# Performance work log

Measured on AMD Instinct MI355X. Metric: run time of the kernel, lower is better.

Reference implementation:

```python
import jax, jax.numpy as jnp
import numpy as np

ALPHA = 1.0
EPS = 1e-6


def setup_inputs() -> dict:
    key = jax.random.key(0)
    ks = jax.random.split(key, 6)
    B, d_lat, hidden, n_genes = 256, 32, 512, 4000
    z = jax.random.normal(ks[0], (B, d_lat), dtype=jnp.float32)
    W1 = jax.random.normal(ks[1], (d_lat, hidden), dtype=jnp.float32) / np.sqrt(d_lat)
    b1 = jnp.zeros((hidden,), dtype=jnp.float32)
    W2 = jax.random.normal(ks[2], (hidden, n_genes), dtype=jnp.float32) / np.sqrt(hidden)
    b2 = jnp.zeros((n_genes,), dtype=jnp.float32)
    log_theta = 0.5 * jax.random.normal(ks[3], (n_genes,), dtype=jnp.float32)
    return {"z": z, "W1": W1, "b1": b1, "W2": W2, "b2": b2, "log_theta": log_theta}


def _decode_mu(z_vec, W1, b1, W2, b2):
    # NB decoder mean for a single latent vector; lib_dummy == 1 so no scaling.
    h = jax.nn.relu(z_vec @ W1 + b1)            # [hidden]
    return jax.nn.softplus(h @ W2 + b2)          # [n_genes]


def reference(z, W1, b1, W2, b2, log_theta):
    d_lat = z.shape[1]
    theta = jnp.exp(log_theta)                   # [G], per-gene dispersion

    f = lambda zv: _decode_mu(zv, W1, b1, W2, b2)

    mu = jax.vmap(f)(z)                          # [B, G]
    J = jax.vmap(jax.jacfwd(f))(z)               # [B, G, d_lat]

    # weights computed under no_grad in the original
    mu_ng = jax.lax.stop_gradient(mu)
    weights = theta / (mu_ng * (mu_ng + theta) + EPS)   # [B, G]

    # Gram[b, i, j] = sum_g J[b,g,i] * w[b,g] * J[b,g,j]  (== U @ U.T with U = sqrt(w)*J^T)
    Gram = jnp.einsum('bgi,bg,bgj->bij', J, weights, J)  # [B, d_lat, d_lat]

    eye = jnp.eye(d_lat, dtype=z.dtype)
    losses = jnp.sum((Gram - ALPHA * eye) ** 2, axis=(1, 2))  # [B]
    return jnp.mean(losses)
```

## Files before the change

### kernel.cpp

```cpp
#include <hip/hip_runtime.h>

typedef __bf16 bf16x8 __attribute__((ext_vector_type(8)));
typedef float f32x4 __attribute__((ext_vector_type(4)));
typedef unsigned short u16x8 __attribute__((ext_vector_type(8)));

typedef const void __attribute__((address_space(1)))* gas_ptr;
typedef void __attribute__((address_space(3)))* las_ptr;

#define GLOAD16(gp, lp) __builtin_amdgcn_global_load_lds((gas_ptr)(gp), (las_ptr)(lp), 16, 0, 0)

__device__ __forceinline__ unsigned short f2bf(float f) {
  unsigned int u = __float_as_uint(f);
  u += 0x7FFF + ((u >> 16) & 1);
  return (unsigned short)(u >> 16);
}
__device__ __forceinline__ float bf2f(unsigned short u) {
  return __uint_as_float(((unsigned int)u) << 16);
}

__global__ __launch_bounds__(256) void k_w2t(const float* __restrict__ W2,
                                             unsigned short* __restrict__ W2T) {
  __shared__ float tile[64][65];
  const int gt = blockIdx.x;
  const int jt = blockIdx.y;
  const int t = threadIdx.x;
  const int c = t & 63, r4 = t >> 6;
#pragma unroll
  for (int r = 0; r < 16; ++r) {
    int jj = r * 4 + r4;
    int g = gt * 64 + c;
    tile[jj][c] = (g < 4000) ? W2[(size_t)(jt * 64 + jj) * 4000 + g] : 0.f;
  }
  __syncthreads();
#pragma unroll
  for (int r = 0; r < 16; ++r) {
    int gg = r * 4 + r4;
    W2T[(size_t)(gt * 64 + gg) * 512 + jt * 64 + c] = f2bf(tile[c][gg]);
  }
}

__global__ __launch_bounds__(256) void k_maskprep(const float* __restrict__ z,
                                                  const float* __restrict__ W1,
                                                  const float* __restrict__ b1,
                                                  unsigned short* __restrict__ Hb,
                                                  unsigned short* __restrict__ Astack) {
  __shared__ float zs[32];
  __shared__ __align__(8) unsigned char mk[512];
  const int b = blockIdx.x, t = threadIdx.x;
  if (t < 32) zs[t] = z[b * 32 + t];
  __syncthreads();
#pragma unroll
  for (int jj = 0; jj < 2; ++jj) {
    int j = t + jj * 256;
    float a = b1[j];
#pragma unroll
    for (int i = 0; i < 32; ++i) a = fmaf(zs[i], W1[i * 512 + j], a);
    bool m = a > 0.f;
    mk[j] = m ? 1 : 0;
    Hb[b * 512 + j] = m ? f2bf(a) : (unsigned short)0;
  }
  __syncthreads();
#pragma unroll
  for (int k = 0; k < 8; ++k) {
    int c8 = t + k * 256;
    int row = c8 >> 6;
    int k8 = (c8 & 63) * 8;
    unsigned long long m8 = *(const unsigned long long*)(mk + k8);
    const float* w = W1 + row * 512 + k8;
    u16x8 out;
#pragma unroll
    for (int e = 0; e < 8; ++e)
      out[e] = ((m8 >> (e * 8)) & 0xffULL) ? f2bf(w[e]) : (unsigned short)0;
    *(u16x8*)(Astack + ((size_t)(b * 32 + row)) * 512 + k8) = out;
  }
}

__global__ __launch_bounds__(512, 2) void k_gemm(const unsigned short* __restrict__ Astack,
                                                 const unsigned short* __restrict__ W2T,
                                                 const unsigned short* __restrict__ Hb,
                                                 const float* __restrict__ b2,
                                                 const float* __restrict__ log_theta,
                                                 float* __restrict__ Gram) {
  extern __shared__ __align__(16) char smem[];

  const int bm = blockIdx.x;
  const int g0 = blockIdx.y * 256;
  const int t = threadIdx.x;
  const int lane = t & 63;
  const int wave = t >> 6;
  const int wm = wave >> 2;
  const int wn = wave & 3;
  const int trow = t >> 3;
  const int kxor = (((t & 7) ^ (trow & 7)) << 3);
  const int c16 = lane & 15;
  const int lg = lane >> 4;

  f32x4 acc[8][4];
#pragma unroll
  for (int mt = 0; mt < 8; ++mt)
#pragma unroll
    for (int nt = 0; nt < 4; ++nt) acc[mt][nt] = (f32x4){0.f, 0.f, 0.f, 0.f};
  f32x4 sacc[4];
#pragma unroll
  for (int nt = 0; nt < 4; ++nt) sacc[nt] = (f32x4){0.f, 0.f, 0.f, 0.f};

  const unsigned short* Aptr = Astack + (size_t)bm * 256 * 512;
  const unsigned short* Bptr = W2T + (size_t)g0 * 512;
  char* H_lds = smem + 139264;

#define STAGE_BIG(buf, kt)                                                            \
  do {                                                                                \
    _Pragma("unroll") for (int q = 0; q < 4; ++q)                                     \
      GLOAD16(Aptr + (size_t)(q * 64 + trow) * 512 + (kt) * 64 + kxor,                \
              smem + (buf) * 65536 + q * 8192 + wave * 1024);                         \
    _Pragma("unroll") for (int q = 0; q < 4; ++q)                                     \
      GLOAD16(Bptr + (size_t)(q * 64 + trow) * 512 + (kt) * 64 + kxor,                \
              smem + (buf) * 65536 + 32768 + q * 8192 + wave * 1024);                 \
  } while (0)

  STAGE_BIG(0, 0);

#pragma unroll
  for (int i = 0; i < 2; ++i) {
    int o = t * 2 + i;
    int row = o >> 6;
    int col8 = (o & 63) * 8;
    u16x8 v;
    if (row < 8) {
      v = *(const u16x8*)(Hb + (size_t)(bm * 8 + row) * 512 + col8);
    } else {
#pragma unroll
      for (int e = 0; e < 8; ++e) v[e] = 0;
    }
    *(u16x8*)(H_lds + row * 1024 + ((col8 * 2) ^ ((row & 7) << 4))) = v;
  }
  __syncthreads();

  for (int kt = 0; kt < 8; ++kt) {
    int cur = kt & 1;
    if (kt < 7) STAGE_BIG(cur ^ 1, kt + 1);
    const char* Ab = smem + cur * 65536;
    const char* Bb = smem + cur * 65536 + 32768;
#pragma unroll
    for (int ks = 0; ks < 2; ++ks) {
      int kb = ks * 64 + lg * 16;
      bf16x8 av[8], bv[4];
#pragma unroll
      for (int mt = 0; mt < 8; ++mt) {
        int row = wm * 128 + mt * 16 + c16;
        av[mt] = *(const bf16x8*)(Ab + row * 128 + (kb ^ ((row & 7) << 4)));
      }
#pragma unroll
      for (int nt = 0; nt < 4; ++nt) {
        int row = wn * 64 + nt * 16 + c16;
        bv[nt] = *(const bf16x8*)(Bb + row * 128 + (kb ^ ((row & 7) << 4)));
      }
#pragma unroll
      for (int mt = 0; mt < 8; ++mt)
#pragma unroll
        for (int nt = 0; nt < 4; ++nt)
          acc[mt][nt] = __builtin_amdgcn_mfma_f32_16x16x32_bf16(av[mt], bv[nt], acc[mt][nt], 0, 0, 0);
      if (wm == 0) {
        bf16x8 hv = *(const bf16x8*)(H_lds + c16 * 1024 +
                                     (((kt * 64 + ks * 32 + lg * 8) * 2) ^ ((c16 & 7) << 4)));
#pragma unroll
        for (int nt = 0; nt < 4; ++nt)
          sacc[nt] = __builtin_amdgcn_mfma_f32_16x16x32_bf16(hv, bv[nt], sacc[nt], 0, 0, 0);
      }
    }
    __syncthreads();
  }

  float* c_lds = (float*)(smem + 131072);

#pragma unroll
  for (int mt = 0; mt < 8; ++mt)
#pragma unroll
    for (int nt = 0; nt < 4; ++nt)
#pragma unroll
      for (int r = 0; r < 4; ++r) {
        int row = wm * 128 + mt * 16 + lg * 4 + r;
        int col = wn * 64 + nt * 16 + c16;
        *(unsigned short*)(smem + row * 512 + ((col * 2) ^ ((row & 7) << 4))) = f2bf(acc[mt][nt][r]);
      }

  if (wm == 0) {
#pragma unroll
    for (int nt = 0; nt < 4; ++nt) {
      int col = wn * 64 + nt * 16 + c16;
      int gg = g0 + col;
      float bb = (gg < 4000) ? b2[gg] : 0.f;
      float th = (gg < 4000) ? expf(log_theta[gg]) : 1.f;
#pragma unroll
      for (int r = 0; r < 4; ++r) {
        int srow = lg * 4 + r;
        if (srow < 8) {
          float s = sacc[nt][r] + bb;
          float sig = 1.f / (1.f + expf(-s));
          float mu = (s > 20.f) ? s : log1pf(expf(s));
          float w = th / (mu * (mu + th) + 1e-6f);
          c_lds[srow * 256 + col] = (gg < 4000) ? (w * sig * sig) : 0.f;
        }
      }
    }
  }
  __syncthreads();

  {
    const int s = wave;
    f32x4 gacc[2][2];
#pragma unroll
    for (int m2 = 0; m2 < 2; ++m2)
#pragma unroll
      for (int n2 = 0; n2 < 2; ++n2) gacc[m2][n2] = (f32x4){0.f, 0.f, 0.f, 0.f};

#pragma unroll
    for (int ch = 0; ch < 8; ++ch) {
      f32x4 cv0 = *(const f32x4*)(c_lds + s * 256 + ch * 32 + lg * 8);
      f32x4 cv1 = *(const f32x4*)(c_lds + s * 256 + ch * 32 + lg * 8 + 4);
      u16x8 raw[2];
      bf16x8 ap[2], bp[2];
#pragma unroll
      for (int m2 = 0; m2 < 2; ++m2) {
        int row = s * 32 + m2 * 16 + c16;
        raw[m2] = *(const u16x8*)(smem + row * 512 + ((ch * 64 + lg * 16) ^ ((row & 7) << 4)));
        u16x8 sc;
#pragma unroll
        for (int e = 0; e < 4; ++e) sc[e] = f2bf(bf2f(raw[m2][e]) * cv0[e]);
#pragma unroll
        for (int e = 0; e < 4; ++e) sc[4 + e] = f2bf(bf2f(raw[m2][4 + e]) * cv1[e]);
        ap[m2] = __builtin_bit_cast(bf16x8, sc);
        bp[m2] = __builtin_bit_cast(bf16x8, raw[m2]);
      }
#pragma unroll
      for (int m2 = 0; m2 < 2; ++m2)
#pragma unroll
        for (int n2 = 0; n2 < 2; ++n2)
          gacc[m2][n2] = __builtin_amdgcn_mfma_f32_16x16x32_bf16(ap[m2], bp[n2], gacc[m2][n2], 0, 0, 0);
    }

#pragma unroll
    for (int m2 = 0; m2 < 2; ++m2)
#pragma unroll
      for (int n2 = 0; n2 < 2; ++n2)
#pragma unroll
        for (int r = 0; r < 4; ++r) {
          int i = m2 * 16 + lg * 4 + r;
          int j = n2 * 16 + c16;
          atomicAdd(Gram + (size_t)(bm * 8 + s) * 1024 + i * 32 + j, gacc[m2][n2][r]);
        }
  }
}

__global__ __launch_bounds__(256) void k_loss(const float* __restrict__ Gram,
                                              float* __restrict__ out) {
  __shared__ float red[4];
  const int b = blockIdx.x, t = threadIdx.x;
  float local = 0.f;
#pragma unroll
  for (int k = 0; k < 4; ++k) {
    int e = t + k * 256;
    float d = Gram[(size_t)b * 1024 + e] - (((e >> 5) == (e & 31)) ? 1.f : 0.f);
    local += d * d;
  }
#pragma unroll
  for (int off = 32; off > 0; off >>= 1) local += __shfl_down(local, off);
  if ((t & 63) == 0) red[t >> 6] = local;
  __syncthreads();
  if (t == 0) {
    float s = red[0] + red[1] + red[2] + red[3];
    atomicAdd(out, s * (1.f / 256.f));
  }
}

extern "C" void kernel_launch(void* const* d_in, const int* in_sizes, int n_in,
                              void* d_out, int out_size, void* d_ws, size_t ws_size,
                              hipStream_t stream) {
  const float* z = (const float*)d_in[0];
  const float* W1 = (const float*)d_in[1];
  const float* b1 = (const float*)d_in[2];
  const float* W2 = (const float*)d_in[3];
  const float* b2 = (const float*)d_in[4];
  const float* lt = (const float*)d_in[5];

  char* ws = (char*)d_ws;
  unsigned short* W2T = (unsigned short*)ws;
  unsigned short* Astack = (unsigned short*)(ws + 4194304);
  unsigned short* Hb = (unsigned short*)(ws + 12582912);
  float* Gram = (float*)(ws + 17170432);

  hipMemsetAsync(Gram, 0, 256 * 1024 * 4, stream);
  hipMemsetAsync(d_out, 0, 4, stream);

  static const int kGemmLds = 139264 + 16384;
  hipFuncSetAttribute((const void*)k_gemm, hipFuncAttributeMaxDynamicSharedMemorySize, kGemmLds);

  k_w2t<<<dim3(64, 8), 256, 0, stream>>>(W2, W2T);
  k_maskprep<<<256, 256, 0, stream>>>(z, W1, b1, Hb, Astack);
  k_gemm<<<dim3(32, 16), 512, kGemmLds, stream>>>(Astack, W2T, Hb, b2, lt, Gram);
  k_loss<<<256, 256, 0, stream>>>(Gram, (float*)d_out);
}
```

Baseline: 149.6 us.

## Merge prep kernels, fold loss into GEMM tail, split H-GEMM across wave rows

The W2 transpose and mask-prep kernels are combined into one launch, with extra grid rows handling the per-sample mask work. The separate loss kernel is removed: the last GEMM block to finish each batch tile, found through an atomic counter, reduces that tile's Gram matrices into the output. The small H·W2 MFMA work is split across both wave rows by k-substep and the partial sums are combined through LDS. This cuts launch count and balances MFMA load between waves, at the cost of an extra LDS sync, threadfences, and a counter reset folded into the memset.

```diff
diff --git a/kernel.cpp b/kernel.cpp
--- a/kernel.cpp
+++ b/kernel.cpp
@@ -18,60 +18,61 @@
   return __uint_as_float(((unsigned int)u) << 16);
 }
 
-__global__ __launch_bounds__(256) void k_w2t(const float* __restrict__ W2,
-                                             unsigned short* __restrict__ W2T) {
+__global__ __launch_bounds__(256) void k_prep(const float* __restrict__ W2,
+                                              unsigned short* __restrict__ W2T,
+                                              const float* __restrict__ z,
+                                              const float* __restrict__ W1,
+                                              const float* __restrict__ b1,
+                                              unsigned short* __restrict__ Hb,
+                                              unsigned short* __restrict__ Astack) {
   __shared__ float tile[64][65];
-  const int gt = blockIdx.x;
-  const int jt = blockIdx.y;
   const int t = threadIdx.x;
-  const int c = t & 63, r4 = t >> 6;
-#pragma unroll
-  for (int r = 0; r < 16; ++r) {
-    int jj = r * 4 + r4;
-    int g = gt * 64 + c;
-    tile[jj][c] = (g < 4000) ? W2[(size_t)(jt * 64 + jj) * 4000 + g] : 0.f;
-  }
-  __syncthreads();
-#pragma unroll
-  for (int r = 0; r < 16; ++r) {
-    int gg = r * 4 + r4;
-    W2T[(size_t)(gt * 64 + gg) * 512 + jt * 64 + c] = f2bf(tile[c][gg]);
-  }
-}
-
-__global__ __launch_bounds__(256) void k_maskprep(const float* __restrict__ z,
-                                                  const float* __restrict__ W1,
-                                                  const float* __restrict__ b1,
-                                                  unsigned short* __restrict__ Hb,
-                                                  unsigned short* __restrict__ Astack) {
-  __shared__ float zs[32];
-  __shared__ __align__(8) unsigned char mk[512];
-  const int b = blockIdx.x, t = threadIdx.x;
-  if (t < 32) zs[t] = z[b * 32 + t];
-  __syncthreads();
-#pragma unroll
-  for (int jj = 0; jj < 2; ++jj) {
-    int j = t + jj * 256;
-    float a = b1[j];
-#pragma unroll
-    for (int i = 0; i < 32; ++i) a = fmaf(zs[i], W1[i * 512 + j], a);
-    bool m = a > 0.f;
-    mk[j] = m ? 1 : 0;
-    Hb[b * 512 + j] = m ? f2bf(a) : (unsigned short)0;
-  }
-  __syncthreads();
-#pragma unroll
-  for (int k = 0; k < 8; ++k) {
-    int c8 = t + k * 256;
-    int row = c8 >> 6;
-    int k8 = (c8 & 63) * 8;
-    unsigned long long m8 = *(const unsigned long long*)(mk + k8);
-    const float* w = W1 + row * 512 + k8;
-    u16x8 out;
-#pragma unroll
-    for (int e = 0; e < 8; ++e)
-      out[e] = ((m8 >> (e * 8)) & 0xffULL) ? f2bf(w[e]) : (unsigned short)0;
-    *(u16x8*)(Astack + ((size_t)(b * 32 + row)) * 512 + k8) = out;
+  if (blockIdx.y < 8) {
+    const int gt = blockIdx.x;
+    const int jt = blockIdx.y;
+    const int c = t & 63, r4 = t >> 6;
+#pragma unroll
+    for (int r = 0; r < 16; ++r) {
+      int jj = r * 4 + r4;
+      int g = gt * 64 + c;
+      tile[jj][c] = (g < 4000) ? W2[(size_t)(jt * 64 + jj) * 4000 + g] : 0.f;
+    }
+    __syncthreads();
+#pragma unroll
+    for (int r = 0; r < 16; ++r) {
+      int gg = r * 4 + r4;
+      W2T[(size_t)(gt * 64 + gg) * 512 + jt * 64 + c] = f2bf(tile[c][gg]);
+    }
+  } else {
+    const int b = blockIdx.x * 4 + (blockIdx.y - 8);
+    float* zs = &tile[0][0];
+    unsigned char* mk = (unsigned char*)&tile[2][0];
+    if (t < 32) zs[t] = z[b * 32 + t];
+    __syncthreads();
+#pragma unroll
+    for (int jj = 0; jj < 2; ++jj) {
+      int j = t + jj * 256;
+      float a = b1[j];
+#pragma unroll
+      for (int i = 0; i < 32; ++i) a = fmaf(zs[i], W1[i * 512 + j], a);
+      bool m = a > 0.f;
+      mk[j] = m ? 1 : 0;
+      Hb[b * 512 + j] = m ? f2bf(a) : (unsigned short)0;
+    }
+    __syncthreads();
+#pragma unroll
+    for (int k = 0; k < 8; ++k) {
+      int c8 = t + k * 256;
+      int row = c8 >> 6;
+      int k8 = (c8 & 63) * 8;
+      unsigned long long m8 = *(const unsigned long long*)(mk + k8);
+      const float* w = W1 + row * 512 + k8;
+      u16x8 out;
+#pragma unroll
+      for (int e = 0; e < 8; ++e)
+        out[e] = ((m8 >> (e * 8)) & 0xffULL) ? f2bf(w[e]) : (unsigned short)0;
+      *(u16x8*)(Astack + ((size_t)(b * 32 + row)) * 512 + k8) = out;
+    }
   }
 }
 
@@ -80,7 +81,9 @@
                                                  const unsigned short* __restrict__ Hb,
                                                  const float* __restrict__ b2,
                                                  const float* __restrict__ log_theta,
-                                                 float* __restrict__ Gram) {
+                                                 float* __restrict__ Gram,
+                                                 int* __restrict__ ctr,
+                                                 float* __restrict__ out) {
   extern __shared__ __align__(16) char smem[];
 
   const int bm = blockIdx.x;
@@ -160,7 +163,7 @@
 #pragma unroll
         for (int nt = 0; nt < 4; ++nt)
           acc[mt][nt] = __builtin_amdgcn_mfma_f32_16x16x32_bf16(av[mt], bv[nt], acc[mt][nt], 0, 0, 0);
-      if (wm == 0) {
+      if (ks == wm) {
         bf16x8 hv = *(const bf16x8*)(H_lds + c16 * 1024 +
                                      (((kt * 64 + ks * 32 + lg * 8) * 2) ^ ((c16 & 7) << 4)));
 #pragma unroll
@@ -185,6 +188,18 @@
       }
 
   if (wm == 0) {
+#pragma unroll
+    for (int nt = 0; nt < 4; ++nt) {
+      int col = wn * 64 + nt * 16 + c16;
+#pragma unroll
+      for (int r = 0; r < 4; ++r) {
+        int srow = lg * 4 + r;
+        if (srow < 8) c_lds[srow * 256 + col] = sacc[nt][r];
+      }
+    }
+  }
+  __syncthreads();
+  if (wm == 1) {
 #pragma unroll
     for (int nt = 0; nt < 4; ++nt) {
       int col = wn * 64 + nt * 16 + c16;
@@ -195,7 +210,7 @@
       for (int r = 0; r < 4; ++r) {
         int srow = lg * 4 + r;
         if (srow < 8) {
-          float s = sacc[nt][r] + bb;
+          float s = sacc[nt][r] + c_lds[srow * 256 + col] + bb;
           float sig = 1.f / (1.f + expf(-s));
           float mu = (s > 20.f) ? s : log1pf(expf(s));
           float w = th / (mu * (mu + th) + 1e-6f);
@@ -250,26 +265,33 @@
           atomicAdd(Gram + (size_t)(bm * 8 + s) * 1024 + i * 32 + j, gacc[m2][n2][r]);
         }
   }
-}
-
-__global__ __launch_bounds__(256) void k_loss(const float* __restrict__ Gram,
-                                              float* __restrict__ out) {
-  __shared__ float red[4];
-  const int b = blockIdx.x, t = threadIdx.x;
-  float local = 0.f;
-#pragma unroll
-  for (int k = 0; k < 4; ++k) {
-    int e = t + k * 256;
-    float d = Gram[(size_t)b * 1024 + e] - (((e >> 5) == (e & 31)) ? 1.f : 0.f);
-    local += d * d;
-  }
-#pragma unroll
-  for (int off = 32; off > 0; off >>= 1) local += __shfl_down(local, off);
-  if ((t & 63) == 0) red[t >> 6] = local;
-  __syncthreads();
-  if (t == 0) {
-    float s = red[0] + red[1] + red[2] + red[3];
-    atomicAdd(out, s * (1.f / 256.f));
+
+  float* red = (float*)(smem + 139264);
+  int* flagp = (int*)(smem + 139264 + 64);
+  __syncthreads();
+  __threadfence();
+  if (t == 0) *flagp = (atomicAdd(ctr + bm, 1) == 15) ? 1 : 0;
+  __syncthreads();
+  if (*flagp) {
+    __threadfence();
+    float local = 0.f;
+#pragma unroll
+    for (int k = 0; k < 16; ++k) {
+      int idx = t + k * 512;
+      int s = idx >> 10, e = idx & 1023;
+      float d = Gram[(size_t)(bm * 8 + s) * 1024 + e] - (((e >> 5) == (e & 31)) ? 1.f : 0.f);
+      local += d * d;
+    }
+#pragma unroll
+    for (int off = 32; off > 0; off >>= 1) local += __shfl_down(local, off);
+    if (lane == 0) red[wave] = local;
+    __syncthreads();
+    if (t == 0) {
+      float s8 = 0.f;
+#pragma unroll
+      for (int w = 0; w < 8; ++w) s8 += red[w];
+      atomicAdd(out, s8 * (1.f / 256.f));
+    }
   }
 }
 
@@ -288,15 +310,15 @@
   unsigned short* Astack = (unsigned short*)(ws + 4194304);
   unsigned short* Hb = (unsigned short*)(ws + 12582912);
   float* Gram = (float*)(ws + 17170432);
-
-  hipMemsetAsync(Gram, 0, 256 * 1024 * 4, stream);
+  int* ctr = (int*)(ws + 18219008);
+
+  hipMemsetAsync(Gram, 0, 1048576 + 128, stream);
   hipMemsetAsync(d_out, 0, 4, stream);
 
   static const int kGemmLds = 139264 + 16384;
   hipFuncSetAttribute((const void*)k_gemm, hipFuncAttributeMaxDynamicSharedMemorySize, kGemmLds);
 
-  k_w2t<<<dim3(64, 8), 256, 0, stream>>>(W2, W2T);
-  k_maskprep<<<256, 256, 0, stream>>>(z, W1, b1, Hb, Astack);
-  k_gemm<<<dim3(32, 16), 512, kGemmLds, stream>>>(Astack, W2T, Hb, b2, lt, Gram);
-  k_loss<<<256, 256, 0, stream>>>(Gram, (float*)d_out);
-}
+  k_prep<<<dim3(64, 12), 256, 0, stream>>>(W2, W2T, z, W1, b1, Hb, Astack);
+  k_gemm<<<dim3(32, 16), 512, kGemmLds, stream>>>(Astack, W2T, Hb, b2, lt, Gram, ctr,
+                                                  (float*)d_out);
+}
```

New measurement: 204.9 us. 37.0% more time.
